# Optimization experiments

Hardware: AMD Instinct MI355X
Metric: run time of the kernel (lower is better)

Reference implementation:

```python
import jax, jax.numpy as jnp
import numpy as np

NB, HD, NL, NF = 5, 64, 4, 10           # num_bins, hidden_dim(d_model), num_layers, num_frames
DI, DS, DC, DTR = 128, 16, 4, 4          # d_inner=2*HD, d_state, d_conv, dt_rank=ceil(HD/16)
B, H, W = 4, 64, 64


def _conv2d(x, w, b):
    y = jax.lax.conv_general_dilated(x, w, (1, 1), 'SAME',
                                     dimension_numbers=('NCHW', 'OIHW', 'NCHW'))
    return y + b[None, :, None, None]


def _bn_relu(x, gamma, beta, eps=1e-5):
    # BatchNorm2d in training mode: biased batch stats over (N,H,W)
    mean = x.mean(axis=(0, 2, 3), keepdims=True)
    var = x.var(axis=(0, 2, 3), keepdims=True)
    y = (x - mean) * jax.lax.rsqrt(var + eps)
    return jax.nn.relu(y * gamma[None, :, None, None] + beta[None, :, None, None])


def _silu(x):
    return x * jax.nn.sigmoid(x)


def _causal_dwconv(x, w, b):
    # x: (B,L,DI), w: (DI,K) depthwise causal conv, b: (DI,)
    K = w.shape[1]
    L = x.shape[1]
    xp = jnp.pad(x, ((0, 0), (K - 1, 0), (0, 0)))
    y = sum(xp[:, k:k + L, :] * w[:, k] for k in range(K))
    return y + b


def _selective_scan(u, delta, A, Bm, Cm, D):
    # u,delta: (B,L,DI); A: (DI,DS); Bm,Cm: (B,L,DS); D: (DI,)
    dT, BT, CT, uT = (t.transpose(1, 0, 2) for t in (delta, Bm, Cm, u))
    h0 = jnp.zeros((u.shape[0], A.shape[0], A.shape[1]), u.dtype)

    def step(h, inp):
        d_t, B_t, C_t, u_t = inp                     # (B,DI),(B,DS),(B,DS),(B,DI)
        dA = jnp.exp(d_t[:, :, None] * A)            # (B,DI,DS)
        h = dA * h + (d_t * u_t)[:, :, None] * B_t[:, None, :]
        y = jnp.einsum('bds,bs->bd', h, C_t)
        return h, y

    _, ys = jax.lax.scan(step, h0, (dT, BT, CT, uT))  # ys: (L,B,DI)
    return ys.transpose(1, 0, 2) + u * D


def _mamba(x, in_proj, conv_w, conv_b, x_proj, dt_w, dt_b, A_log, Dp, out_proj):
    xz = x @ in_proj.T                               # (B,L,2*DI)
    xi, z = jnp.split(xz, 2, axis=-1)
    xi = _silu(_causal_dwconv(xi, conv_w, conv_b))
    xdbc = xi @ x_proj.T                             # (B,L,DTR+2*DS)
    dt, Bm, Cm = jnp.split(xdbc, [DTR, DTR + DS], axis=-1)
    delta = jax.nn.softplus(dt @ dt_w.T + dt_b)
    A = -jnp.exp(A_log)
    y = _selective_scan(xi, delta, A, Bm, Cm, Dp)
    return (y * _silu(z)) @ out_proj.T


def setup_inputs() -> dict:
    key = jax.random.key(0)
    ks = jax.random.split(key, 20)
    s = 0.02
    inp = {
        'x': jax.random.normal(ks[0], (B, NB, H, W), jnp.float32),
        'enc_w': jax.random.normal(ks[1], (HD, NB, 3, 3), jnp.float32) * s,
        'enc_b': jnp.zeros((HD,), jnp.float32),
        'enc_g': jnp.ones((HD,), jnp.float32),
        'enc_be': jnp.zeros((HD,), jnp.float32),
        'in_proj': jax.random.normal(ks[2], (NL, 2 * DI, HD), jnp.float32) * s,
        'conv_w': jax.random.normal(ks[3], (NL, DI, DC), jnp.float32) * s,
        'conv_b': jnp.zeros((NL, DI), jnp.float32),
        'x_proj': jax.random.normal(ks[4], (NL, DTR + 2 * DS, DI), jnp.float32) * s,
        'dt_w': jax.random.normal(ks[5], (NL, DI, DTR), jnp.float32) * s,
        'dt_b': jax.random.normal(ks[6], (NL, DI), jnp.float32) * 0.1 - 4.0,
        'A_log': jnp.broadcast_to(jnp.log(jnp.arange(1, DS + 1, dtype=jnp.float32)),
                                  (NL, DI, DS)).copy(),
        'Dp': jnp.ones((NL, DI), jnp.float32),
        'out_proj': jax.random.normal(ks[7], (NL, HD, DI), jnp.float32) * s,
        'dec1_w': jax.random.normal(ks[8], (HD, HD, 3, 3), jnp.float32) * s,
        'dec1_b': jnp.zeros((HD,), jnp.float32),
        'dec1_g': jnp.ones((HD,), jnp.float32),
        'dec1_be': jnp.zeros((HD,), jnp.float32),
        'dec2_w': jax.random.normal(ks[9], (NF, HD, 3, 3), jnp.float32) * s,
        'dec2_b': jnp.zeros((NF,), jnp.float32),
    }
    return inp


def reference(x, enc_w, enc_b, enc_g, enc_be, in_proj, conv_w, conv_b, x_proj,
              dt_w, dt_b, A_log, Dp, out_proj, dec1_w, dec1_b, dec1_g, dec1_be,
              dec2_w, dec2_b):
    Bb, _, Hh, Ww = x.shape
    h = _bn_relu(_conv2d(x, enc_w, enc_b), enc_g, enc_be)   # (B,HD,H,W)
    t = h.reshape(Bb, HD, Hh * Ww).transpose(0, 2, 1)        # (B,L,HD)
    for i in range(NL):
        t = t + _mamba(t, in_proj[i], conv_w[i], conv_b[i], x_proj[i],
                       dt_w[i], dt_b[i], A_log[i], Dp[i], out_proj[i])
    h = t.transpose(0, 2, 1).reshape(Bb, HD, Hh, Ww)
    h = _bn_relu(_conv2d(h, dec1_w, dec1_b), dec1_g, dec1_be)
    return _conv2d(h, dec2_w, dec2_b)                        # (B,NF,H,W)
```

## Files before the change

### kernel.cpp

```cpp
#include <hip/hip_runtime.h>
#include <hip/hip_bf16.h>

#define BB   4
#define NBC  5
#define HD   64
#define NLAYER 4
#define NFC  10
#define DIM  128
#define DSN  16
#define DCN  4
#define DTRK 4
#define HH   64
#define WWD  64
#define LL   4096
#define MM   (BB*LL)
#define NCHUNK 128
#define CLEN   32
#define TSTEP  16

__global__ void k_enc_conv(const float* __restrict__ x, const float* __restrict__ w,
                           const float* __restrict__ bias, float* __restrict__ out) {
    int idx = blockIdx.x * blockDim.x + threadIdx.x;
    int wx = idx & 63;
    int hy = (idx >> 6) & 63;
    int co = (idx >> 12) & 63;
    int b  = idx >> 18;
    float acc = bias[co];
    for (int ci = 0; ci < NBC; ++ci) {
        const float* xin = x + (((long)(b * NBC + ci)) << 12);
        const float* wp  = w + (co * NBC + ci) * 9;
        #pragma unroll
        for (int kh = 0; kh < 3; ++kh) {
            int ih = hy + kh - 1;
            if (ih < 0 || ih >= HH) continue;
            #pragma unroll
            for (int kw = 0; kw < 3; ++kw) {
                int iw = wx + kw - 1;
                if (iw < 0 || iw >= WWD) continue;
                acc += xin[(ih << 6) + iw] * wp[kh * 3 + kw];
            }
        }
    }
    out[idx] = acc;
}

__global__ void k_bn_stats(const float* __restrict__ src, float* __restrict__ mv) {
    __shared__ float s1[256];
    __shared__ float s2[256];
    int c = blockIdx.x;
    int tid = threadIdx.x;
    float sum = 0.f, sq = 0.f;
    for (int i = tid; i < BB * LL; i += 256) {
        int b = i >> 12;
        int hw = i & 4095;
        float v = src[((long)((b << 6) + c) << 12) + hw];
        sum += v; sq += v * v;
    }
    s1[tid] = sum; s2[tid] = sq;
    __syncthreads();
    for (int off = 128; off > 0; off >>= 1) {
        if (tid < off) { s1[tid] += s1[tid + off]; s2[tid] += s2[tid + off]; }
        __syncthreads();
    }
    if (tid == 0) {
        float m = s1[0] * (1.f / 16384.f);
        mv[c] = m;
        mv[64 + c] = s2[0] * (1.f / 16384.f) - m * m;
    }
}

__global__ void k_bn_tr_seq(const float* __restrict__ src, const float* __restrict__ mv,
                            const float* __restrict__ g, const float* __restrict__ be,
                            float* __restrict__ tout) {
    __shared__ float s[64 * 65];
    int blk = blockIdx.x;
    int b = blk >> 6;
    int hw0 = (blk & 63) << 6;
    int tid = threadIdx.x;
    for (int i = tid; i < 4096; i += 256) {
        int pix = i & 63, c = i >> 6;
        s[c * 65 + pix] = src[((long)((b << 6) + c) << 12) + hw0 + pix];
    }
    __syncthreads();
    for (int i = tid; i < 4096; i += 256) {
        int c = i & 63, pix = i >> 6;
        float v = s[c * 65 + pix];
        float y = (v - mv[c]) * rsqrtf(mv[64 + c] + 1e-5f) * g[c] + be[c];
        tout[((long)((b << 12) + hw0 + pix) << 6) + c] = fmaxf(y, 0.f);
    }
}

__global__ void k_bn_stats_pm_part(const float* __restrict__ src, float* __restrict__ pbuf) {
    __shared__ float s1[256], s2[256];
    int g = blockIdx.x;
    int tid = threadIdx.x;
    int c = tid & 63;
    int p = tid >> 6;
    float sum = 0.f, sq = 0.f;
    for (int row = (g << 2) + p; row < MM; row += 256) {
        float v = src[(long)row * 64 + c];
        sum += v; sq += v * v;
    }
    s1[tid] = sum; s2[tid] = sq;
    __syncthreads();
    if (p == 0) {
        sum = s1[c] + s1[64 + c] + s1[128 + c] + s1[192 + c];
        sq  = s2[c] + s2[64 + c] + s2[128 + c] + s2[192 + c];
        pbuf[(g << 6) + c] = sum;
        pbuf[4096 + (g << 6) + c] = sq;
    }
}

__global__ void k_bn_stats_pm_fin(const float* __restrict__ pbuf, float* __restrict__ mv) {
    int c = threadIdx.x;
    float s = 0.f, q = 0.f;
    for (int g = 0; g < 64; ++g) {
        s += pbuf[(g << 6) + c];
        q += pbuf[4096 + (g << 6) + c];
    }
    float m = s * (1.f / 16384.f);
    mv[c] = m;
    mv[64 + c] = q * (1.f / 16384.f) - m * m;
}

__global__ void k_prep_wt(const float* __restrict__ in_proj, const float* __restrict__ out_proj,
                          float* __restrict__ wTin, float* __restrict__ wTout) {
    int idx = blockIdx.x * blockDim.x + threadIdx.x;
    if (idx < 65536) {
        int n = idx & 255, k = (idx >> 8) & 63, l = idx >> 14;
        wTin[idx] = in_proj[(l << 14) + (n << 6) + k];
    } else {
        int j = idx - 65536;
        int n = j & 63, k = (j >> 6) & 127, l = j >> 13;
        wTout[j] = out_proj[(l << 13) + (n << 7) + k];
    }
}

__global__ __launch_bounds__(256, 1) void k_gemm_in2(const float* __restrict__ tin,
                                                     const float* __restrict__ wT,
                                                     float* __restrict__ xz) {
    __shared__ __align__(16) float ts[64 * 68];
    long m0 = (long)blockIdx.x << 6;
    int tid = threadIdx.x;
    int rg = tid >> 5;
    int cg = tid & 31;
    for (int i = tid; i < 4096; i += 256) {
        int r = i >> 6, k = i & 63;
        ts[r * 68 + k] = tin[(m0 << 6) + i];
    }
    __syncthreads();
    float acc[8][8] = {};
    int n0 = cg << 3;
    for (int k4 = 0; k4 < 16; ++k4) {
        float4 a[8];
        #pragma unroll
        for (int r2 = 0; r2 < 8; ++r2)
            a[r2] = *(const float4*)&ts[((rg << 3) + r2) * 68 + (k4 << 2)];
        #pragma unroll
        for (int kk = 0; kk < 4; ++kk) {
            const float* wr = wT + (((k4 << 2) + kk) << 8) + n0;
            float4 w0 = *(const float4*)&wr[0];
            float4 w1 = *(const float4*)&wr[4];
            #pragma unroll
            for (int r2 = 0; r2 < 8; ++r2) {
                float av = (kk == 0) ? a[r2].x : (kk == 1) ? a[r2].y
                         : (kk == 2) ? a[r2].z : a[r2].w;
                acc[r2][0] += av * w0.x; acc[r2][1] += av * w0.y;
                acc[r2][2] += av * w0.z; acc[r2][3] += av * w0.w;
                acc[r2][4] += av * w1.x; acc[r2][5] += av * w1.y;
                acc[r2][6] += av * w1.z; acc[r2][7] += av * w1.w;
            }
        }
    }
    #pragma unroll
    for (int r2 = 0; r2 < 8; ++r2) {
        long m = m0 + (rg << 3) + r2;
        *(float4*)&xz[(m << 8) + n0]     = make_float4(acc[r2][0], acc[r2][1], acc[r2][2], acc[r2][3]);
        *(float4*)&xz[(m << 8) + n0 + 4] = make_float4(acc[r2][4], acc[r2][5], acc[r2][6], acc[r2][7]);
    }
}

__global__ void k_xproj_fused(const float* __restrict__ xz, const float* __restrict__ cw,
                              const float* __restrict__ cb, const float* __restrict__ Wx,
                              const float* __restrict__ dw, const float* __restrict__ dbias,
                              float* __restrict__ xi, float* __restrict__ xdbc,
                              float* __restrict__ delta) {
    __shared__ float xz_s[35 * 132];
    __shared__ float xi_s[32 * 132];
    __shared__ float w_s[36 * 132];
    __shared__ float xs[32 * 40];
    __shared__ float cwT[4 * 128];
    __shared__ float cb_s[128];
    long m0 = (long)blockIdx.x << 5;
    int l0 = (int)(m0 & 4095);
    int tid = threadIdx.x;

    for (int i = tid; i < 35 * 128; i += 256) {
        int j = i >> 7, k = i & 127;
        int l = l0 - 3 + j;
        float v = 0.f;
        if (l >= 0) v = xz[(m0 - 3 + j) * 256 + k];
        xz_s[j * 132 + k] = v;
    }
    if (tid < 128) cb_s[tid] = cb[tid];
    for (int i = tid; i < 512; i += 256) {
        int kk = i >> 7, di = i & 127;
        cwT[(kk << 7) + di] = cw[(di << 2) + kk];
    }
    for (int i = tid; i < 4608; i += 256) {
        int n = i >> 7, k = i & 127;
        w_s[n * 132 + k] = Wx[i];
// ... 21 lines not shown
    }
    __syncthreads();

    int n = tid & 63;
    int rg = tid >> 6;
    if (n < 36) {
        float acc[8] = {0,0,0,0,0,0,0,0};
        for (int k4 = 0; k4 < 32; ++k4) {
            float4 w4 = *(const float4*)&w_s[n * 132 + (k4 << 2)];
            #pragma unroll
            for (int r = 0; r < 8; ++r) {
                float4 a4 = *(const float4*)&xi_s[((rg << 3) + r) * 132 + (k4 << 2)];
                acc[r] += a4.x * w4.x + a4.y * w4.y + a4.z * w4.z + a4.w * w4.w;
            }
        }
        #pragma unroll
        for (int r = 0; r < 8; ++r) {
            int rr = (rg << 3) + r;
            xdbc[(m0 + rr) * 36 + n] = acc[r];
            xs[rr * 40 + n] = acc[r];
        }
    }
    __syncthreads();
    for (int i = tid; i < 4096; i += 256) {
        int r = i >> 7, di = i & 127;
        float v = dbias[di];
        float4 d4 = *(const float4*)&dw[di << 2];
        v += xs[r * 40 + 0] * d4.x + xs[r * 40 + 1] * d4.y
           + xs[r * 40 + 2] * d4.z + xs[r * 40 + 3] * d4.w;
        delta[(m0 + r) * 128 + di] = (v > 20.f) ? v : log1pf(expf(v));
    }
}

__global__ void k_scan_p1(const float* __restrict__ delta, const float* __restrict__ xi,
                          const float* __restrict__ xdbc, const float* __restrict__ A_log,
                          float* __restrict__ Pb, float* __restrict__ Sb) {
    __shared__ float d_s[TSTEP][64];
    __shared__ float u_s[TSTEP][64];
    __shared__ float b_s[TSTEP][16];
    int chunk = blockIdx.x, b = blockIdx.y, half = blockIdx.z;
    int tid = threadIdx.x;
    int dq = tid & 3;
    int dil = tid >> 2;
    int di = (half << 6) + dil;
    float4 al = *(const float4*)&A_log[(di << 4) + (dq << 2)];
    float Av[4] = { -expf(al.x), -expf(al.y), -expf(al.z), -expf(al.w) };
    float h[4] = {0.f, 0.f, 0.f, 0.f};
    float P[4] = {1.f, 1.f, 1.f, 1.f};
    long t0 = ((long)b << 12) + (long)chunk * CLEN;

    int srow = tid >> 4, sc4 = (tid & 15) << 2;
    for (int tile = 0; tile < CLEN / TSTEP; ++tile) {
        __syncthreads();
        long ls = t0 + tile * TSTEP + srow;
        *(float4*)&d_s[srow][sc4] = *(const float4*)&delta[(ls << 7) + (half << 6) + sc4];
        *(float4*)&u_s[srow][sc4] = *(const float4*)&xi[(ls << 7) + (half << 6) + sc4];
        if (tid < 64) {
            int r2 = tid >> 2, cc = (tid & 3) << 2;
            long l2 = t0 + tile * TSTEP + r2;
            *(float4*)&b_s[r2][cc] = *(const float4*)&xdbc[l2 * 36 + DTRK + cc];
        }
        __syncthreads();
        #pragma unroll
        for (int i = 0; i < TSTEP; ++i) {
            float d = d_s[i][dil];
            float u = u_s[i][dil];
            float du = d * u;
            float4 Bv = *(float4*)&b_s[i][dq << 2];
            float a0 = __expf(d * Av[0]); h[0] = a0 * h[0] + du * Bv.x; P[0] *= a0;
            float a1 = __expf(d * Av[1]); h[1] = a1 * h[1] + du * Bv.y; P[1] *= a1;
            float a2 = __expf(d * Av[2]); h[2] = a2 * h[2] + du * Bv.z; P[2] *= a2;
            float a3 = __expf(d * Av[3]); h[3] = a3 * h[3] + du * Bv.w; P[3] *= a3;
        }
    }
    long o = (((long)chunk * BB + b) << 11) + (di << 4) + (dq << 2);
    *(float4*)&Pb[o] = make_float4(P[0], P[1], P[2], P[3]);
    *(float4*)&Sb[o] = make_float4(h[0], h[1], h[2], h[3]);
}

__global__ void k_scan_p2(float* Pb, const float* __restrict__ Sb) {
    int t = blockIdx.x * blockDim.x + threadIdx.x;
    int b = t >> 11;
    int s = t & 2047;
    float h = 0.f;
    for (int c = 0; c < NCHUNK; ++c) {
        long idx = (((long)c * BB + b) << 11) + s;
        float p = Pb[idx];
        float sv = Sb[idx];
        Pb[idx] = h;
        h = p * h + sv;
    }
}

__global__ void k_scan_p3(const float* __restrict__ delta, const float* __restrict__ xi,
                          const float* __restrict__ xdbc, const float* __restrict__ A_log,
                          const float* __restrict__ Dp, const float* __restrict__ xz,
                          const float* __restrict__ hin, float* __restrict__ gated) {
    __shared__ float d_s[TSTEP][64];
    __shared__ float u_s[TSTEP][64];
    __shared__ float bc_s[TSTEP][32];
    __shared__ float y_s[TSTEP][64];
    int chunk = blockIdx.x, b = blockIdx.y, half = blockIdx.z;
    int tid = threadIdx.x;
    int dq = tid & 3;
    int dil = tid >> 2;
    int di = (half << 6) + dil;
    float4 al = *(const float4*)&A_log[(di << 4) + (dq << 2)];
    float Av[4] = { -expf(al.x), -expf(al.y), -expf(al.z), -expf(al.w) };
    float Dv = Dp[di];
    long ho = (((long)chunk * BB + b) << 11) + (di << 4) + (dq << 2);
    float4 h4 = *(const float4*)&hin[ho];
    float h[4] = { h4.x, h4.y, h4.z, h4.w };
    long t0 = ((long)b << 12) + (long)chunk * CLEN;

    int srow = tid >> 4, sc4 = (tid & 15) << 2;
    for (int tile = 0; tile < CLEN / TSTEP; ++tile) {
        __syncthreads();
        long ls = t0 + tile * TSTEP + srow;
        *(float4*)&d_s[srow][sc4] = *(const float4*)&delta[(ls << 7) + (half << 6) + sc4];
        *(float4*)&u_s[srow][sc4] = *(const float4*)&xi[(ls << 7) + (half << 6) + sc4];
        if (tid < 128) {
            int r2 = tid >> 3, cc = (tid & 7) << 2;
            long l2 = t0 + tile * TSTEP + r2;
            *(float4*)&bc_s[r2][cc] = *(const float4*)&xdbc[l2 * 36 + DTRK + cc];
        }
        __syncthreads();
        #pragma unroll
        for (int i = 0; i < TSTEP; ++i) {
            float d = d_s[i][dil];
            float u = u_s[i][dil];
            float du = d * u;
            float4 Bv = *(float4*)&bc_s[i][dq << 2];
            float4 Cv = *(float4*)&bc_s[i][16 + (dq << 2)];
            float a0 = __expf(d * Av[0]); h[0] = a0 * h[0] + du * Bv.x;
            float a1 = __expf(d * Av[1]); h[1] = a1 * h[1] + du * Bv.y;
            float a2 = __expf(d * Av[2]); h[2] = a2 * h[2] + du * Bv.z;
            float a3 = __expf(d * Av[3]); h[3] = a3 * h[3] + du * Bv.w;
            float yp = h[0] * Cv.x + h[1] * Cv.y + h[2] * Cv.z + h[3] * Cv.w;
            yp += __shfl_xor(yp, 1);
            yp += __shfl_xor(yp, 2);
            if (dq == 0)
                y_s[i][dil] = yp + u * Dv;
        }
        __syncthreads();
        {
            long l = t0 + tile * TSTEP + srow;
            float4 y4 = *(float4*)&y_s[srow][sc4];
            float4 z4 = *(const float4*)&xz[(l << 8) + DIM + (half << 6) + sc4];
            float4 o;
            o.x = y4.x * (z4.x / (1.f + __expf(-z4.x)));
            o.y = y4.y * (z4.y / (1.f + __expf(-z4.y)));
            o.z = y4.z * (z4.z / (1.f + __expf(-z4.z)));
            o.w = y4.w * (z4.w / (1.f + __expf(-z4.w)));
            *(float4*)&gated[(l << 7) + (half << 6) + sc4] = o;
        }
    }
}

__global__ __launch_bounds__(256, 1) void k_gemm_out2(const float* __restrict__ gated,
                                                      const float* __restrict__ wT,
                                                      float* __restrict__ tio) {
    __shared__ __align__(16) float ts[64 * 132];
    long m0 = (long)blockIdx.x << 6;
    int tid = threadIdx.x;
    int rg = tid >> 4;
    int cg = tid & 15;
    for (int i = tid; i < 8192; i += 256) {
        int r2 = i >> 7, k = i & 127;
        ts[r2 * 132 + k] = gated[(m0 << 7) + i];
    }
    __syncthreads();
    float acc[4][4] = {};
    int n0 = cg << 2;
    for (int k4 = 0; k4 < 32; ++k4) {
        float4 a[4];
        #pragma unroll
        for (int r2 = 0; r2 < 4; ++r2)
            a[r2] = *(const float4*)&ts[((rg << 2) + r2) * 132 + (k4 << 2)];
        #pragma unroll
        for (int kk = 0; kk < 4; ++kk) {
            const float* wr = wT + (((k4 << 2) + kk) << 6) + n0;
            float4 w0 = *(const float4*)&wr[0];
            #pragma unroll
            for (int r2 = 0; r2 < 4; ++r2) {
                float av = (kk == 0) ? a[r2].x : (kk == 1) ? a[r2].y
                         : (kk == 2) ? a[r2].z : a[r2].w;
                acc[r2][0] += av * w0.x; acc[r2][1] += av * w0.y;
                acc[r2][2] += av * w0.z; acc[r2][3] += av * w0.w;
            }
        }
    }
    #pragma unroll
    for (int r2 = 0; r2 < 4; ++r2) {
        long m = m0 + (rg << 2) + r2;
        float4 t0 = *(const float4*)&tio[(m << 6) + n0];
        t0.x += acc[r2][0]; t0.y += acc[r2][1];
        t0.z += acc[r2][2]; t0.w += acc[r2][3];
        *(float4*)&tio[(m << 6) + n0] = t0;
    }
}

__global__ void k_prep_wdec1(const float* __restrict__ w, float* __restrict__ wT) {
    int idx = blockIdx.x * blockDim.x + threadIdx.x;
    int co = idx & 63;
    int tap = (idx >> 6) % 9;
    int ci = idx / 576;
    wT[idx] = w[co * 576 + ci * 9 + tap];
}

__global__ void k_prep_wdec2(const float* __restrict__ w, float* __restrict__ wT) {
    int idx = blockIdx.x * blockDim.x + threadIdx.x;
    if (idx >= 64 * NFC * 12) return;
    int tap = idx % 12;
    int t2 = idx / 12;
    int co = t2 % NFC;
    int ci = t2 / NFC;
    wT[idx] = (tap < 9) ? w[co * 576 + ci * 9 + tap] : 0.f;
}

__global__ __launch_bounds__(256, 1) void k_dec1_new(const float* __restrict__ tin,
                                                     const float* __restrict__ wT,
                                                     const float* __restrict__ bias,
                                                     float* __restrict__ out) {
    __shared__ __align__(16) float x_s[64 * 132];
    __shared__ __align__(16) float w_s[4 * 4608];
    int tile = blockIdx.x;
    int b = blockIdx.y;
    int ty0 = (tile >> 3) << 3;
    int tx0 = (tile & 7) << 3;
    int tid = threadIdx.x;
    int wv = tid >> 6;
    int lane = tid & 63;
    int r = lane >> 3;
    int cg = lane & 7;

    for (int i = tid; i < 6400; i += 256) {
        int pl = i >> 6;
        int c = i & 63;
        int py = pl / 10, px = pl - py * 10;
        int ih = ty0 + py - 1, iw = tx0 + px - 1;
        float v = 0.f;
        if (ih >= 0 && ih < HH && iw >= 0 && iw < WWD)
            v = tin[(((long)((b << 12) + (ih << 6) + iw)) << 6) + c];
        x_s[c * 132 + py * 12 + px] = v;
    }
    float* myw = &w_s[wv * 4608];
    const float* gw = wT + (wv * 16) * 576;
    float4 pref[18];
    #pragma unroll
    for (int i = 0; i < 18; ++i)
        pref[i] = *(const float4*)&gw[(i * 64 + lane) * 4];
    #pragma unroll
    for (int i = 0; i < 18; ++i)
        *(float4*)&myw[(i * 64 + lane) * 4] = pref[i];
    __syncthreads();

// ... 23 lines not shown
            #pragma unroll
            for (int kh = 0; kh < 3; ++kh) {
                #pragma unroll
                for (int kw = 0; kw < 3; ++kw) {
                    const float* wp2 = wp + (kh * 3 + kw) * 64 + (cg << 3);
                    float4 wa = *(const float4*)&wp2[0];
                    float4 wb = *(const float4*)&wp2[4];
                    #pragma unroll
                    for (int j = 0; j < 8; ++j) {
                        float xv = xrow[kh][kw + j];
                        acc[j][0] += xv * wa.x; acc[j][1] += xv * wa.y;
                        acc[j][2] += xv * wa.z; acc[j][3] += xv * wa.w;
                        acc[j][4] += xv * wb.x; acc[j][5] += xv * wb.y;
                        acc[j][6] += xv * wb.z; acc[j][7] += xv * wb.w;
                    }
                }
            }
        }
        if (ch == 0) {
            #pragma unroll
            for (int i = 0; i < 18; ++i)
                *(float4*)&myw[(i * 64 + lane) * 4] = pref[i];
        }
    }

    #pragma unroll
    for (int j = 0; j < 8; ++j) {
        *(float4*)&myw[lane * 68 + (j << 3)]     = make_float4(acc[j][0], acc[j][1], acc[j][2], acc[j][3]);
        *(float4*)&myw[lane * 68 + (j << 3) + 4] = make_float4(acc[j][4], acc[j][5], acc[j][6], acc[j][7]);
    }
    __syncthreads();

    float bv = bias[lane];
    #pragma unroll
    for (int pp = 0; pp < 16; ++pp) {
        int pr = (wv << 1) + (pp >> 3);
        int pc = pp & 7;
        int ol = (pr << 3) + (lane >> 3);
        int ix = (pc << 3) + (lane & 7);
        float s = w_s[ol * 68 + ix] + w_s[4608 + ol * 68 + ix]
                + w_s[9216 + ol * 68 + ix] + w_s[13824 + ol * 68 + ix] + bv;
        out[(((long)((b << 12) + ((ty0 + pr) << 6) + tx0 + pc)) << 6) + lane] = s;
    }
}

__global__ void k_dec2_fused(const float* __restrict__ src, const float* __restrict__ mv,
                             const float* __restrict__ g, const float* __restrict__ be,
                             const float* __restrict__ wT, const float* __restrict__ bias,
                             float* __restrict__ out) {
    __shared__ float x_s[64 * 101];
    __shared__ float w_s[64 * NFC * 12];
    __shared__ float sc_s[64];
    __shared__ float sh_s[64];
    int tile = blockIdx.x;
    int b = blockIdx.y;
    int ty0 = (tile >> 3) << 3;
    int tx0 = (tile & 7) << 3;
    int tid = threadIdx.x;

    if (tid < 64) {
        float m = mv[tid], v = mv[64 + tid];
        float s = g[tid] * rsqrtf(v + 1e-5f);
        sc_s[tid] = s;
        sh_s[tid] = be[tid] - m * s;
    }
    for (int i = tid; i < 64 * NFC * 12; i += 256)
        w_s[i] = wT[i];
    __syncthreads();

    for (int i = tid; i < 6400; i += 256) {
        int pl = i >> 6;
        int c = i & 63;
        int py = pl / 10, px = pl - py * 10;
        int ih = ty0 + py - 1, iw = tx0 + px - 1;
        float v = 0.f;
        if (ih >= 0 && ih < HH && iw >= 0 && iw < WWD) {
            v = src[((long)((b << 12) + (ih << 6) + iw)) * 64 + c];
            v = fmaxf(v * sc_s[c] + sh_s[c], 0.f);
        }
        x_s[c * 101 + pl] = v;
    }
    __syncthreads();

    int px = tid & 63;
    int py = px >> 3, pxx = px & 7;
    int cog = tid >> 6;
    float acc[3] = {0.f, 0.f, 0.f};
    int nco = (cog < 2) ? 3 : 2;

    for (int ci = 0; ci < 64; ++ci) {
        const float* xr = &x_s[ci * 101 + py * 10 + pxx];
        float xv[9];
        #pragma unroll
        for (int kh = 0; kh < 3; ++kh)
            #pragma unroll
// ... 19 lines not shown
        int co = cog + (j << 2);
        out[((long)(b * NFC + co) << 12) + hw] = acc[j] + bias[co];
    }
}

extern "C" void kernel_launch(void* const* d_in, const int* in_sizes, int n_in,
                              void* d_out, int out_size, void* d_ws, size_t ws_size,
                              hipStream_t stream) {
    const float* x       = (const float*)d_in[0];
    const float* enc_w   = (const float*)d_in[1];
    const float* enc_b   = (const float*)d_in[2];
    const float* enc_g   = (const float*)d_in[3];
    const float* enc_be  = (const float*)d_in[4];
    const float* in_proj = (const float*)d_in[5];
    const float* conv_w  = (const float*)d_in[6];
    const float* conv_b  = (const float*)d_in[7];
    const float* x_proj  = (const float*)d_in[8];
    const float* dt_w    = (const float*)d_in[9];
    const float* dt_b    = (const float*)d_in[10];
    const float* A_log   = (const float*)d_in[11];
    const float* Dp      = (const float*)d_in[12];
    const float* out_prj = (const float*)d_in[13];
    const float* dec1_w  = (const float*)d_in[14];
    const float* dec1_b  = (const float*)d_in[15];
    const float* dec1_g  = (const float*)d_in[16];
    const float* dec1_be = (const float*)d_in[17];
    const float* dec2_w  = (const float*)d_in[18];
    const float* dec2_b  = (const float*)d_in[19];
    float* out = (float*)d_out;

    float* ws = (float*)d_ws;
    size_t off = 0;
    float* conv_buf  = ws + off; off += 1048576;
    float* mv        = ws + off; off += 128;
    float* pbuf      = ws + off; off += 8192;
    float* wT1       = ws + off; off += 36864;
    float* wT2       = ws + off; off += 7680;
    float* wTin      = ws + off; off += 65536;
    float* wTout     = ws + off; off += 32768;
    float* t_buf     = ws + off; off += 1048576;
    float* xz_buf    = ws + off; off += 4194304;
    float* xi_buf    = ws + off; off += 2097152;
    float* xdbc_buf  = ws + off; off += 589824;
    float* delta_buf = ws + off; off += 2097152;
    float* gated_buf = ws + off; off += 2097152;
    (void)ws_size; (void)in_sizes; (void)n_in; (void)out_size;

    float* Pb = conv_buf;
    float* Sb = gated_buf;

    k_prep_wt<<<384, 256, 0, stream>>>(in_proj, out_prj, wTin, wTout);
    k_prep_wdec1<<<144, 256, 0, stream>>>(dec1_w, wT1);
    k_prep_wdec2<<<30, 256, 0, stream>>>(dec2_w, wT2);

    k_enc_conv<<<4096, 256, 0, stream>>>(x, enc_w, enc_b, conv_buf);
    k_bn_stats<<<64, 256, 0, stream>>>(conv_buf, mv);
    k_bn_tr_seq<<<256, 256, 0, stream>>>(conv_buf, mv, enc_g, enc_be, t_buf);

    dim3 sg(NCHUNK, BB, 2);
    for (int i = 0; i < NLAYER; ++i) {
        k_gemm_in2<<<256, 256, 0, stream>>>(t_buf, wTin + i * 16384, xz_buf);
        k_xproj_fused<<<512, 256, 0, stream>>>(xz_buf, conv_w + i * DIM * DCN,
                                               conv_b + i * DIM, x_proj + i * 36 * DIM,
                                               dt_w + i * DIM * DTRK, dt_b + i * DIM,
                                               xi_buf, xdbc_buf, delta_buf);
        k_scan_p1<<<sg, 256, 0, stream>>>(delta_buf, xi_buf, xdbc_buf,
                                          A_log + i * DIM * DSN, Pb, Sb);
        k_scan_p2<<<32, 256, 0, stream>>>(Pb, Sb);
        k_scan_p3<<<sg, 256, 0, stream>>>(delta_buf, xi_buf, xdbc_buf,
                                          A_log + i * DIM * DSN, Dp + i * DIM,
                                          xz_buf, Pb, gated_buf);
        k_gemm_out2<<<256, 256, 0, stream>>>(gated_buf, wTout + i * 8192, t_buf);
    }

    dim3 dg1(64, BB);
    k_dec1_new<<<dg1, 256, 0, stream>>>(t_buf, wT1, dec1_b, conv_buf);
    k_bn_stats_pm_part<<<64, 256, 0, stream>>>(conv_buf, pbuf);
    k_bn_stats_pm_fin<<<1, 64, 0, stream>>>(pbuf, mv);
    k_dec2_fused<<<dg1, 256, 0, stream>>>(conv_buf, mv, dec1_g, dec1_be, wT2, dec2_b, out);
}
```

Baseline: 565.8 us.

## Fuse scan phases with grid barriers, fold BN stats into convs, merge GEMMs

Merges the three selective-scan kernels into one persistent kernel that uses atomic-counter grid barriers, so it relies on all 1024 blocks being co-resident. Batch-norm statistics are now accumulated with atomics inside the encoder and dec1 convolutions, which removes separate reduction passes. The out-projection GEMM is fused with the next layer's in-projection GEMM, and the weight-prep kernels are merged into one. The goal is fewer launches and less global traffic. The risks are deadlock if occupancy falls short, contention on the atomics, and run-to-run differences in float summation order.

```diff
diff --git a/kernel.cpp b/kernel.cpp
--- a/kernel.cpp
+++ b/kernel.cpp
@@ -17,10 +17,56 @@
 #define NCHUNK 128
 #define CLEN   32
 #define TSTEP  16
+#define NBLK_SCAN 1024
+
+__device__ __forceinline__ void gbar(int* c, int n) {
+    __threadfence();
+    __syncthreads();
+    if (threadIdx.x == 0) {
+        atomicAdd(c, 1);
+        while (atomicAdd(c, 0) < n)
+            __builtin_amdgcn_s_sleep(16);
+        __threadfence();
+    }
+    __syncthreads();
+}
+
+__global__ void k_prep_all(const float* __restrict__ in_proj, const float* __restrict__ out_proj,
+                           const float* __restrict__ dec1_w, const float* __restrict__ dec2_w,
+                           float* __restrict__ wTin, float* __restrict__ wTout,
+                           float* __restrict__ wT1, float* __restrict__ wT2,
+                           float* __restrict__ stats, float* __restrict__ stats2,
+                           int* __restrict__ sync) {
+    int idx = blockIdx.x * blockDim.x + threadIdx.x;
+    if (idx < 65536) {
+        int n = idx & 255, k = (idx >> 8) & 63, l = idx >> 14;
+        wTin[idx] = in_proj[(l << 14) + (n << 6) + k];
+    } else if (idx < 98304) {
+        int j = idx - 65536;
+        int n = j & 63, k = (j >> 6) & 127, l = j >> 13;
+        wTout[j] = out_proj[(l << 13) + (n << 7) + k];
+    } else if (idx < 135168) {
+        int j = idx - 98304;
+        int co = j & 63, tap = (j >> 6) % 9, ci = j / 576;
+        wT1[j] = dec1_w[co * 576 + ci * 9 + tap];
+    } else if (idx < 142848) {
+        int j = idx - 135168;
+        int tap = j % 12, t2 = j / 12, co = t2 % NFC, ci = t2 / NFC;
+        wT2[j] = (tap < 9) ? dec2_w[co * 576 + ci * 9 + tap] : 0.f;
+    } else if (idx < 143104) {
+        int j = idx - 142848;
+        if (j < 128) stats[j] = 0.f; else stats2[j - 128] = 0.f;
+    } else if (idx < 143168) {
+        sync[idx - 143104] = 0;
+    }
+}
 
 __global__ void k_enc_conv(const float* __restrict__ x, const float* __restrict__ w,
-                           const float* __restrict__ bias, float* __restrict__ out) {
-    int idx = blockIdx.x * blockDim.x + threadIdx.x;
+                           const float* __restrict__ bias, float* __restrict__ out,
+                           float* __restrict__ stats) {
+    __shared__ float r1[256], r2[256];
+    int tid = threadIdx.x;
+    int idx = blockIdx.x * 256 + tid;
     int wx = idx & 63;
     int hy = (idx >> 6) & 63;
     int co = (idx >> 12) & 63;
@@ -42,41 +88,33 @@
         }
     }
     out[idx] = acc;
-}
-
-__global__ void k_bn_stats(const float* __restrict__ src, float* __restrict__ mv) {
-    __shared__ float s1[256];
-    __shared__ float s2[256];
-    int c = blockIdx.x;
-    int tid = threadIdx.x;
-    float sum = 0.f, sq = 0.f;
-    for (int i = tid; i < BB * LL; i += 256) {
-        int b = i >> 12;
-        int hw = i & 4095;
-        float v = src[((long)((b << 6) + c) << 12) + hw];
-        sum += v; sq += v * v;
-    }
-    s1[tid] = sum; s2[tid] = sq;
+    r1[tid] = acc; r2[tid] = acc * acc;
     __syncthreads();
     for (int off = 128; off > 0; off >>= 1) {
-        if (tid < off) { s1[tid] += s1[tid + off]; s2[tid] += s2[tid + off]; }
+        if (tid < off) { r1[tid] += r1[tid + off]; r2[tid] += r2[tid + off]; }
         __syncthreads();
     }
     if (tid == 0) {
-        float m = s1[0] * (1.f / 16384.f);
-        mv[c] = m;
-        mv[64 + c] = s2[0] * (1.f / 16384.f) - m * m;
-    }
-}
-
-__global__ void k_bn_tr_seq(const float* __restrict__ src, const float* __restrict__ mv,
+        atomicAdd(&stats[co], r1[0]);
+        atomicAdd(&stats[64 + co], r2[0]);
+    }
+}
+
+__global__ void k_bn_tr_seq(const float* __restrict__ src, const float* __restrict__ stats,
                             const float* __restrict__ g, const float* __restrict__ be,
                             float* __restrict__ tout) {
     __shared__ float s[64 * 65];
+    __shared__ float sc[64], sh[64];
     int blk = blockIdx.x;
     int b = blk >> 6;
     int hw0 = (blk & 63) << 6;
     int tid = threadIdx.x;
+    if (tid < 64) {
+        float m = stats[tid] * (1.f / 16384.f);
+        float var = stats[64 + tid] * (1.f / 16384.f) - m * m;
+        float ss = g[tid] * rsqrtf(var + 1e-5f);
+        sc[tid] = ss; sh[tid] = be[tid] - m * ss;
+    }
     for (int i = tid; i < 4096; i += 256) {
         int pix = i & 63, c = i >> 6;
         s[c * 65 + pix] = src[((long)((b << 6) + c) << 12) + hw0 + pix];
@@ -84,55 +122,8 @@
     __syncthreads();
     for (int i = tid; i < 4096; i += 256) {
         int c = i & 63, pix = i >> 6;
-        float v = s[c * 65 + pix];
-        float y = (v - mv[c]) * rsqrtf(mv[64 + c] + 1e-5f) * g[c] + be[c];
+        float y = s[c * 65 + pix] * sc[c] + sh[c];
         tout[((long)((b << 12) + hw0 + pix) << 6) + c] = fmaxf(y, 0.f);
-    }
-}
-
-__global__ void k_bn_stats_pm_part(const float* __restrict__ src, float* __restrict__ pbuf) {
-    __shared__ float s1[256], s2[256];
-    int g = blockIdx.x;
-    int tid = threadIdx.x;
-    int c = tid & 63;
-    int p = tid >> 6;
-    float sum = 0.f, sq = 0.f;
-    for (int row = (g << 2) + p; row < MM; row += 256) {
-        float v = src[(long)row * 64 + c];
-        sum += v; sq += v * v;
-    }
-    s1[tid] = sum; s2[tid] = sq;
-    __syncthreads();
-    if (p == 0) {
-        sum = s1[c] + s1[64 + c] + s1[128 + c] + s1[192 + c];
-        sq  = s2[c] + s2[64 + c] + s2[128 + c] + s2[192 + c];
-        pbuf[(g << 6) + c] = sum;
-        pbuf[4096 + (g << 6) + c] = sq;
-    }
-}
-
-__global__ void k_bn_stats_pm_fin(const float* __restrict__ pbuf, float* __restrict__ mv) {
-    int c = threadIdx.x;
-    float s = 0.f, q = 0.f;
-    for (int g = 0; g < 64; ++g) {
-        s += pbuf[(g << 6) + c];
-        q += pbuf[4096 + (g << 6) + c];
-    }
-    float m = s * (1.f / 16384.f);
-    mv[c] = m;
-    mv[64 + c] = q * (1.f / 16384.f) - m * m;
-}
-
-__global__ void k_prep_wt(const float* __restrict__ in_proj, const float* __restrict__ out_proj,
-                          float* __restrict__ wTin, float* __restrict__ wTout) {
-    int idx = blockIdx.x * blockDim.x + threadIdx.x;
-    if (idx < 65536) {
-        int n = idx & 255, k = (idx >> 8) & 63, l = idx >> 14;
-        wTin[idx] = in_proj[(l << 14) + (n << 6) + k];
-    } else {
-        int j = idx - 65536;
-        int n = j & 63, k = (j >> 6) & 127, l = j >> 13;
-        wTout[j] = out_proj[(l << 13) + (n << 7) + k];
     }
 }
 
@@ -177,6 +168,130 @@
         long m = m0 + (rg << 3) + r2;
         *(float4*)&xz[(m << 8) + n0]     = make_float4(acc[r2][0], acc[r2][1], acc[r2][2], acc[r2][3]);
         *(float4*)&xz[(m << 8) + n0 + 4] = make_float4(acc[r2][4], acc[r2][5], acc[r2][6], acc[r2][7]);
+    }
+}
+
+__global__ __launch_bounds__(256, 1) void k_gemm_oi(const float* __restrict__ gated,
+                                                    const float* __restrict__ wTo,
+                                                    const float* __restrict__ wTi,
+                                                    float* __restrict__ tio,
+                                                    float* __restrict__ xz) {
+    __shared__ __align__(16) float g_s[64 * 132];
+    __shared__ __align__(16) float t_s[64 * 68];
+    long m0 = (long)blockIdx.x << 6;
+    int tid = threadIdx.x;
+    for (int i = tid; i < 8192; i += 256) {
+        int r = i >> 7, k = i & 127;
+        g_s[r * 132 + k] = gated[(m0 << 7) + i];
+    }
+    __syncthreads();
+    {
+        int rg = tid >> 4, cg = tid & 15;
+        int n0 = cg << 2;
+        float acc[4][4] = {};
+        for (int k4 = 0; k4 < 32; ++k4) {
+            float4 a[4];
+            #pragma unroll
+            for (int r2 = 0; r2 < 4; ++r2)
+                a[r2] = *(const float4*)&g_s[((rg << 2) + r2) * 132 + (k4 << 2)];
+            #pragma unroll
+            for (int kk = 0; kk < 4; ++kk) {
+                const float* wr = wTo + (((k4 << 2) + kk) << 6) + n0;
+                float4 w0 = *(const float4*)&wr[0];
+                #pragma unroll
+                for (int r2 = 0; r2 < 4; ++r2) {
+                    float av = (kk == 0) ? a[r2].x : (kk == 1) ? a[r2].y
+                             : (kk == 2) ? a[r2].z : a[r2].w;
+                    acc[r2][0] += av * w0.x; acc[r2][1] += av * w0.y;
+                    acc[r2][2] += av * w0.z; acc[r2][3] += av * w0.w;
+                }
+            }
+        }
+        #pragma unroll
+        for (int r2 = 0; r2 < 4; ++r2) {
+            long m = m0 + (rg << 2) + r2;
+            float4 t0 = *(const float4*)&tio[(m << 6) + n0];
+            t0.x += acc[r2][0]; t0.y += acc[r2][1];
+            t0.z += acc[r2][2]; t0.w += acc[r2][3];
+            *(float4*)&tio[(m << 6) + n0] = t0;
+            *(float4*)&t_s[((rg << 2) + r2) * 68 + n0] = t0;
+        }
+    }
+    __syncthreads();
+    {
+        int rg = tid >> 5, cg = tid & 31;
+        int n0 = cg << 3;
+        float acc[8][8] = {};
+        for (int k4 = 0; k4 < 16; ++k4) {
+            float4 a[8];
+            #pragma unroll
+            for (int r2 = 0; r2 < 8; ++r2)
+                a[r2] = *(const float4*)&t_s[((rg << 3) + r2) * 68 + (k4 << 2)];
+            #pragma unroll
+            for (int kk = 0; kk < 4; ++kk) {
+                const float* wr = wTi + (((k4 << 2) + kk) << 8) + n0;
+                float4 w0 = *(const float4*)&wr[0];
+                float4 w1 = *(const float4*)&wr[4];
+                #pragma unroll
+                for (int r2 = 0; r2 < 8; ++r2) {
+                    float av = (kk == 0) ? a[r2].x : (kk == 1) ? a[r2].y
+                             : (kk == 2) ? a[r2].z : a[r2].w;
+                    acc[r2][0] += av * w0.x; acc[r2][1] += av * w0.y;
+                    acc[r2][2] += av * w0.z; acc[r2][3] += av * w0.w;
+                    acc[r2][4] += av * w1.x; acc[r2][5] += av * w1.y;
+                    acc[r2][6] += av * w1.z; acc[r2][7] += av * w1.w;
+                }
+            }
+        }
+        #pragma unroll
+        for (int r2 = 0; r2 < 8; ++r2) {
+            long m = m0 + (rg << 3) + r2;
+            *(float4*)&xz[(m << 8) + n0]     = make_float4(acc[r2][0], acc[r2][1], acc[r2][2], acc[r2][3]);
+            *(float4*)&xz[(m << 8) + n0 + 4] = make_float4(acc[r2][4], acc[r2][5], acc[r2][6], acc[r2][7]);
+        }
+    }
+}
+
+__global__ __launch_bounds__(256, 1) void k_gemm_out2(const float* __restrict__ gated,
+                                                      const float* __restrict__ wT,
+                                                      float* __restrict__ tio) {
+    __shared__ __align__(16) float ts[64 * 132];
+    long m0 = (long)blockIdx.x << 6;
+    int tid = threadIdx.x;
+    int rg = tid >> 4;
+    int cg = tid & 15;
+    for (int i = tid; i < 8192; i += 256) {
+        int r2 = i >> 7, k = i & 127;
+        ts[r2 * 132 + k] = gated[(m0 << 7) + i];
+    }
+    __syncthreads();
+    float acc[4][4] = {};
+    int n0 = cg << 2;
+    for (int k4 = 0; k4 < 32; ++k4) {
+        float4 a[4];
+        #pragma unroll
+        for (int r2 = 0; r2 < 4; ++r2)
+            a[r2] = *(const float4*)&ts[((rg << 2) + r2) * 132 + (k4 << 2)];
+        #pragma unroll
+        for (int kk = 0; kk < 4; ++kk) {
+            const float* wr = wT + (((k4 << 2) + kk) << 6) + n0;
+            float4 w0 = *(const float4*)&wr[0];
+            #pragma unroll
+            for (int r2 = 0; r2 < 4; ++r2) {
+                float av = (kk == 0) ? a[r2].x : (kk == 1) ? a[r2].y
+                         : (kk == 2) ? a[r2].z : a[r2].w;
+                acc[r2][0] += av * w0.x; acc[r2][1] += av * w0.y;
+                acc[r2][2] += av * w0.z; acc[r2][3] += av * w0.w;
+            }
+        }
+    }
+    #pragma unroll
+    for (int r2 = 0; r2 < 4; ++r2) {
+        long m = m0 + (rg << 2) + r2;
+        float4 t0 = *(const float4*)&tio[(m << 6) + n0];
+        t0.x += acc[r2][0]; t0.y += acc[r2][1];
+        t0.z += acc[r2][2]; t0.w += acc[r2][3];
+        *(float4*)&tio[(m << 6) + n0] = t0;
     }
 }
 
@@ -264,12 +379,15 @@
     }
 }
 
-__global__ void k_scan_p1(const float* __restrict__ delta, const float* __restrict__ xi,
-                          const float* __restrict__ xdbc, const float* __restrict__ A_log,
-                          float* __restrict__ Pb, float* __restrict__ Sb) {
+__global__ __launch_bounds__(256, 4) void k_scan(
+        const float* __restrict__ delta, const float* __restrict__ xi,
+        const float* __restrict__ xdbc, const float* __restrict__ A_log,
+        const float* __restrict__ Dp, const float* __restrict__ xz,
+        float* Pb, float* Sb, float* __restrict__ gated, int* sync) {
     __shared__ float d_s[TSTEP][64];
     __shared__ float u_s[TSTEP][64];
-    __shared__ float b_s[TSTEP][16];
+    __shared__ float bc_s[TSTEP][32];
+    __shared__ float y_s[TSTEP][64];
     int chunk = blockIdx.x, b = blockIdx.y, half = blockIdx.z;
     int tid = threadIdx.x;
     int dq = tid & 3;
@@ -277,183 +395,112 @@
     int di = (half << 6) + dil;
     float4 al = *(const float4*)&A_log[(di << 4) + (dq << 2)];
     float Av[4] = { -expf(al.x), -expf(al.y), -expf(al.z), -expf(al.w) };
-    float h[4] = {0.f, 0.f, 0.f, 0.f};
-    float P[4] = {1.f, 1.f, 1.f, 1.f};
     long t0 = ((long)b << 12) + (long)chunk * CLEN;
-
     int srow = tid >> 4, sc4 = (tid & 15) << 2;
-    for (int tile = 0; tile < CLEN / TSTEP; ++tile) {
-        __syncthreads();
-        long ls = t0 + tile * TSTEP + srow;
-        *(float4*)&d_s[srow][sc4] = *(const float4*)&delta[(ls << 7) + (half << 6) + sc4];
-        *(float4*)&u_s[srow][sc4] = *(const float4*)&xi[(ls << 7) + (half << 6) + sc4];
-        if (tid < 64) {
-            int r2 = tid >> 2, cc = (tid & 3) << 2;
-            long l2 = t0 + tile * TSTEP + r2;
-            *(float4*)&b_s[r2][cc] = *(const float4*)&xdbc[l2 * 36 + DTRK + cc];
-        }
-        __syncthreads();
-        #pragma unroll
-        for (int i = 0; i < TSTEP; ++i) {
-            float d = d_s[i][dil];
-            float u = u_s[i][dil];
-            float du = d * u;
-            float4 Bv = *(float4*)&b_s[i][dq << 2];
-            float a0 = __expf(d * Av[0]); h[0] = a0 * h[0] + du * Bv.x; P[0] *= a0;
-            float a1 = __expf(d * Av[1]); h[1] = a1 * h[1] + du * Bv.y; P[1] *= a1;
-            float a2 = __expf(d * Av[2]); h[2] = a2 * h[2] + du * Bv.z; P[2] *= a2;
-            float a3 = __expf(d * Av[3]); h[3] = a3 * h[3] + du * Bv.w; P[3] *= a3;
-        }
-    }
     long o = (((long)chunk * BB + b) << 11) + (di << 4) + (dq << 2);
-    *(float4*)&Pb[o] = make_float4(P[0], P[1], P[2], P[3]);
-    *(float4*)&Sb[o] = make_float4(h[0], h[1], h[2], h[3]);
-}
-
-__global__ void k_scan_p2(float* Pb, const float* __restrict__ Sb) {
-    int t = blockIdx.x * blockDim.x + threadIdx.x;
-    int b = t >> 11;
-    int s = t & 2047;
-    float h = 0.f;
-    for (int c = 0; c < NCHUNK; ++c) {
-        long idx = (((long)c * BB + b) << 11) + s;
-        float p = Pb[idx];
-        float sv = Sb[idx];
-        Pb[idx] = h;
-        h = p * h + sv;
-    }
-}
-
-__global__ void k_scan_p3(const float* __restrict__ delta, const float* __restrict__ xi,
-                          const float* __restrict__ xdbc, const float* __restrict__ A_log,
-                          const float* __restrict__ Dp, const float* __restrict__ xz,
-                          const float* __restrict__ hin, float* __restrict__ gated) {
-    __shared__ float d_s[TSTEP][64];
-    __shared__ float u_s[TSTEP][64];
-    __shared__ float bc_s[TSTEP][32];
-    __shared__ float y_s[TSTEP][64];
-    int chunk = blockIdx.x, b = blockIdx.y, half = blockIdx.z;
-    int tid = threadIdx.x;
-    int dq = tid & 3;
-    int dil = tid >> 2;
-    int di = (half << 6) + dil;
-    float4 al = *(const float4*)&A_log[(di << 4) + (dq << 2)];
-    float Av[4] = { -expf(al.x), -expf(al.y), -expf(al.z), -expf(al.w) };
-    float Dv = Dp[di];
-    long ho = (((long)chunk * BB + b) << 11) + (di << 4) + (dq << 2);
-    float4 h4 = *(const float4*)&hin[ho];
-    float h[4] = { h4.x, h4.y, h4.z, h4.w };
-    long t0 = ((long)b << 12) + (long)chunk * CLEN;
-
-    int srow = tid >> 4, sc4 = (tid & 15) << 2;
-    for (int tile = 0; tile < CLEN / TSTEP; ++tile) {
-        __syncthreads();
-        long ls = t0 + tile * TSTEP + srow;
-        *(float4*)&d_s[srow][sc4] = *(const float4*)&delta[(ls << 7) + (half << 6) + sc4];
-        *(float4*)&u_s[srow][sc4] = *(const float4*)&xi[(ls << 7) + (half << 6) + sc4];
-        if (tid < 128) {
-            int r2 = tid >> 3, cc = (tid & 7) << 2;
-            long l2 = t0 + tile * TSTEP + r2;
-            *(float4*)&bc_s[r2][cc] = *(const float4*)&xdbc[l2 * 36 + DTRK + cc];
-        }
-        __syncthreads();
-        #pragma unroll
-        for (int i = 0; i < TSTEP; ++i) {
-            float d = d_s[i][dil];
-            float u = u_s[i][dil];
-            float du = d * u;
-            float4 Bv = *(float4*)&bc_s[i][dq << 2];
-            float4 Cv = *(float4*)&bc_s[i][16 + (dq << 2)];
-            float a0 = __expf(d * Av[0]); h[0] = a0 * h[0] + du * Bv.x;
-            float a1 = __expf(d * Av[1]); h[1] = a1 * h[1] + du * Bv.y;
-            float a2 = __expf(d * Av[2]); h[2] = a2 * h[2] + du * Bv.z;
-            float a3 = __expf(d * Av[3]); h[3] = a3 * h[3] + du * Bv.w;
-            float yp = h[0] * Cv.x + h[1] * Cv.y + h[2] * Cv.z + h[3] * Cv.w;
-            yp += __shfl_xor(yp, 1);
-            yp += __shfl_xor(yp, 2);
-            if (dq == 0)
-                y_s[i][dil] = yp + u * Dv;
-        }
-        __syncthreads();
-        {
-            long l = t0 + tile * TSTEP + srow;
-            float4 y4 = *(float4*)&y_s[srow][sc4];
-            float4 z4 = *(const float4*)&xz[(l << 8) + DIM + (half << 6) + sc4];
-            float4 o;
-            o.x = y4.x * (z4.x / (1.f + __expf(-z4.x)));
-            o.y = y4.y * (z4.y / (1.f + __expf(-z4.y)));
-            o.z = y4.z * (z4.z / (1.f + __expf(-z4.z)));
-            o.w = y4.w * (z4.w / (1.f + __expf(-z4.w)));
-            *(float4*)&gated[(l << 7) + (half << 6) + sc4] = o;
-        }
-    }
-}
-
-__global__ __launch_bounds__(256, 1) void k_gemm_out2(const float* __restrict__ gated,
-                                                      const float* __restrict__ wT,
-                                                      float* __restrict__ tio) {
-    __shared__ __align__(16) float ts[64 * 132];
-    long m0 = (long)blockIdx.x << 6;
-    int tid = threadIdx.x;
-    int rg = tid >> 4;
-    int cg = tid & 15;
-    for (int i = tid; i < 8192; i += 256) {
-        int r2 = i >> 7, k = i & 127;
-        ts[r2 * 132 + k] = gated[(m0 << 7) + i];
-    }
-    __syncthreads();
-    float acc[4][4] = {};
-    int n0 = cg << 2;
-    for (int k4 = 0; k4 < 32; ++k4) {
-        float4 a[4];
-        #pragma unroll
-        for (int r2 = 0; r2 < 4; ++r2)
-            a[r2] = *(const float4*)&ts[((rg << 2) + r2) * 132 + (k4 << 2)];
-        #pragma unroll
-        for (int kk = 0; kk < 4; ++kk) {
-            const float* wr = wT + (((k4 << 2) + kk) << 6) + n0;
-            float4 w0 = *(const float4*)&wr[0];
-            #pragma unroll
-            for (int r2 = 0; r2 < 4; ++r2) {
-                float av = (kk == 0) ? a[r2].x : (kk == 1) ? a[r2].y
-                         : (kk == 2) ? a[r2].z : a[r2].w;
-                acc[r2][0] += av * w0.x; acc[r2][1] += av * w0.y;
-                acc[r2][2] += av * w0.z; acc[r2][3] += av * w0.w;
-            }
-        }
-    }
-    #pragma unroll
-    for (int r2 = 0; r2 < 4; ++r2) {
-        long m = m0 + (rg << 2) + r2;
-        float4 t0 = *(const float4*)&tio[(m << 6) + n0];
-        t0.x += acc[r2][0]; t0.y += acc[r2][1];
-        t0.z += acc[r2][2]; t0.w += acc[r2][3];
-        *(float4*)&tio[(m << 6) + n0] = t0;
-    }
-}
-
-__global__ void k_prep_wdec1(const float* __restrict__ w, float* __restrict__ wT) {
-    int idx = blockIdx.x * blockDim.x + threadIdx.x;
-    int co = idx & 63;
-    int tap = (idx >> 6) % 9;
-    int ci = idx / 576;
-    wT[idx] = w[co * 576 + ci * 9 + tap];
-}
-
-__global__ void k_prep_wdec2(const float* __restrict__ w, float* __restrict__ wT) {
-    int idx = blockIdx.x * blockDim.x + threadIdx.x;
-    if (idx >= 64 * NFC * 12) return;
-    int tap = idx % 12;
-    int t2 = idx / 12;
-    int co = t2 % NFC;
-    int ci = t2 / NFC;
-    wT[idx] = (tap < 9) ? w[co * 576 + ci * 9 + tap] : 0.f;
+
+    {
+        float h[4] = {0.f, 0.f, 0.f, 0.f};
+        float P[4] = {1.f, 1.f, 1.f, 1.f};
+        for (int tile = 0; tile < CLEN / TSTEP; ++tile) {
+            __syncthreads();
+            long ls = t0 + tile * TSTEP + srow;
+            *(float4*)&d_s[srow][sc4] = *(const float4*)&delta[(ls << 7) + (half << 6) + sc4];
+            *(float4*)&u_s[srow][sc4] = *(const float4*)&xi[(ls << 7) + (half << 6) + sc4];
+            if (tid < 64) {
+                int r2 = tid >> 2, cc = (tid & 3) << 2;
+                long l2 = t0 + tile * TSTEP + r2;
+                *(float4*)&bc_s[r2][cc] = *(const float4*)&xdbc[l2 * 36 + DTRK + cc];
+            }
+            __syncthreads();
+            #pragma unroll
+            for (int i = 0; i < TSTEP; ++i) {
+                float d = d_s[i][dil];
+                float u = u_s[i][dil];
+                float du = d * u;
+                float4 Bv = *(float4*)&bc_s[i][dq << 2];
+                float a0 = __expf(d * Av[0]); h[0] = a0 * h[0] + du * Bv.x; P[0] *= a0;
+                float a1 = __expf(d * Av[1]); h[1] = a1 * h[1] + du * Bv.y; P[1] *= a1;
+                float a2 = __expf(d * Av[2]); h[2] = a2 * h[2] + du * Bv.z; P[2] *= a2;
+                float a3 = __expf(d * Av[3]); h[3] = a3 * h[3] + du * Bv.w; P[3] *= a3;
+            }
+        }
+        *(float4*)&Pb[o] = make_float4(P[0], P[1], P[2], P[3]);
+        *(float4*)&Sb[o] = make_float4(h[0], h[1], h[2], h[3]);
+    }
+    gbar(sync, NBLK_SCAN);
+
+    {
+        int flat = blockIdx.x + (blockIdx.y << 7) + (blockIdx.z << 9);
+        if (flat < 32) {
+            int t = (flat << 8) + tid;
+            int bb = t >> 11;
+            int s = t & 2047;
+            float h = 0.f;
+            for (int c = 0; c < NCHUNK; ++c) {
+                long idx2 = (((long)c * BB + bb) << 11) + s;
+                float p = Pb[idx2];
+                float sv = Sb[idx2];
+                Pb[idx2] = h;
+                h = p * h + sv;
+            }
+        }
+    }
+    gbar(sync + 1, NBLK_SCAN);
+
+    {
+        float Dv = Dp[di];
+        float4 h4 = *(const float4*)&Pb[o];
+        float h[4] = { h4.x, h4.y, h4.z, h4.w };
+        for (int tile = 0; tile < CLEN / TSTEP; ++tile) {
+            __syncthreads();
+            long ls = t0 + tile * TSTEP + srow;
+            *(float4*)&d_s[srow][sc4] = *(const float4*)&delta[(ls << 7) + (half << 6) + sc4];
+            *(float4*)&u_s[srow][sc4] = *(const float4*)&xi[(ls << 7) + (half << 6) + sc4];
+            if (tid < 128) {
+                int r2 = tid >> 3, cc = (tid & 7) << 2;
+                long l2 = t0 + tile * TSTEP + r2;
+                *(float4*)&bc_s[r2][cc] = *(const float4*)&xdbc[l2 * 36 + DTRK + cc];
+            }
+            __syncthreads();
+            #pragma unroll
+            for (int i = 0; i < TSTEP; ++i) {
+                float d = d_s[i][dil];
+                float u = u_s[i][dil];
+                float du = d * u;
+                float4 Bv = *(float4*)&bc_s[i][dq << 2];
+                float4 Cv = *(float4*)&bc_s[i][16 + (dq << 2)];
+                float a0 = __expf(d * Av[0]); h[0] = a0 * h[0] + du * Bv.x;
+                float a1 = __expf(d * Av[1]); h[1] = a1 * h[1] + du * Bv.y;
+                float a2 = __expf(d * Av[2]); h[2] = a2 * h[2] + du * Bv.z;
+                float a3 = __expf(d * Av[3]); h[3] = a3 * h[3] + du * Bv.w;
+                float yp = h[0] * Cv.x + h[1] * Cv.y + h[2] * Cv.z + h[3] * Cv.w;
+                yp += __shfl_xor(yp, 1);
+                yp += __shfl_xor(yp, 2);
+                if (dq == 0)
+                    y_s[i][dil] = yp + u * Dv;
+            }
+            __syncthreads();
+            {
+                long l = t0 + tile * TSTEP + srow;
+                float4 y4 = *(float4*)&y_s[srow][sc4];
+                float4 z4 = *(const float4*)&xz[(l << 8) + DIM + (half << 6) + sc4];
+                float4 og;
+                og.x = y4.x * (z4.x / (1.f + __expf(-z4.x)));
+                og.y = y4.y * (z4.y / (1.f + __expf(-z4.y)));
+                og.z = y4.z * (z4.z / (1.f + __expf(-z4.z)));
+                og.w = y4.w * (z4.w / (1.f + __expf(-z4.w)));
+                *(float4*)&gated[(l << 7) + (half << 6) + sc4] = og;
+            }
+        }
+    }
 }
 
 __global__ __launch_bounds__(256, 1) void k_dec1_new(const float* __restrict__ tin,
                                                      const float* __restrict__ wT,
                                                      const float* __restrict__ bias,
-                                                     float* __restrict__ out) {
+                                                     float* __restrict__ out,
+                                                     float* __restrict__ stats2) {
     __shared__ __align__(16) float x_s[64 * 132];
     __shared__ __align__(16) float w_s[4 * 4608];
     int tile = blockIdx.x;
@@ -543,6 +590,7 @@
     __syncthreads();
 
     float bv = bias[lane];
+    float ssum = 0.f, ssq = 0.f;
     #pragma unroll
     for (int pp = 0; pp < 16; ++pp) {
         int pr = (wv << 1) + (pp >> 3);
@@ -552,10 +600,21 @@
         float s = w_s[ol * 68 + ix] + w_s[4608 + ol * 68 + ix]
                 + w_s[9216 + ol * 68 + ix] + w_s[13824 + ol * 68 + ix] + bv;
         out[(((long)((b << 12) + ((ty0 + pr) << 6) + tx0 + pc)) << 6) + lane] = s;
-    }
-}
-
-__global__ void k_dec2_fused(const float* __restrict__ src, const float* __restrict__ mv,
+        ssum += s; ssq += s * s;
+    }
+    float* red = x_s;
+    red[(wv << 6) + lane] = ssum;
+    red[256 + (wv << 6) + lane] = ssq;
+    __syncthreads();
+    if (tid < 64) {
+        float a = red[tid] + red[64 + tid] + red[128 + tid] + red[192 + tid];
+        float q = red[256 + tid] + red[320 + tid] + red[384 + tid] + red[448 + tid];
+        atomicAdd(&stats2[tid], a);
+        atomicAdd(&stats2[64 + tid], q);
+    }
+}
+
+__global__ void k_dec2_fused(const float* __restrict__ src, const float* __restrict__ stats2,
                              const float* __restrict__ g, const float* __restrict__ be,
                              const float* __restrict__ wT, const float* __restrict__ bias,
                              float* __restrict__ out) {
@@ -570,8 +629,9 @@
     int tid = threadIdx.x;
 
     if (tid < 64) {
-        float m = mv[tid], v = mv[64 + tid];
-        float s = g[tid] * rsqrtf(v + 1e-5f);
+        float m = stats2[tid] * (1.f / 16384.f);
+        float var = stats2[64 + tid] * (1.f / 16384.f) - m * m;
+        float s = g[tid] * rsqrtf(var + 1e-5f);
         sc_s[tid] = s;
         sh_s[tid] = be[tid] - m * s;
     }
@@ -657,8 +717,9 @@
     float* ws = (float*)d_ws;
     size_t off = 0;
     float* conv_buf  = ws + off; off += 1048576;
-    float* mv        = ws + off; off += 128;
-    float* pbuf      = ws + off; off += 8192;
+    float* stats     = ws + off; off += 128;
+    float* stats2    = ws + off; off += 128;
+    float* syncf     = ws + off; off += 64;
     float* wT1       = ws + off; off += 36864;
     float* wT2       = ws + off; off += 7680;
     float* wTin      = ws + off; off += 65536;
@@ -671,36 +732,33 @@
     float* gated_buf = ws + off; off += 2097152;
     (void)ws_size; (void)in_sizes; (void)n_in; (void)out_size;
 
+    int* syncbuf = (int*)syncf;
     float* Pb = conv_buf;
     float* Sb = gated_buf;
 
-    k_prep_wt<<<384, 256, 0, stream>>>(in_proj, out_prj, wTin, wTout);
-    k_prep_wdec1<<<144, 256, 0, stream>>>(dec1_w, wT1);
-    k_prep_wdec2<<<30, 256, 0, stream>>>(dec2_w, wT2);
-
-    k_enc_conv<<<4096, 256, 0, stream>>>(x, enc_w, enc_b, conv_buf);
-    k_bn_stats<<<64, 256, 0, stream>>>(conv_buf, mv);
-    k_bn_tr_seq<<<256, 256, 0, stream>>>(conv_buf, mv, enc_g, enc_be, t_buf);
+    k_prep_all<<<560, 256, 0, stream>>>(in_proj, out_prj, dec1_w, dec2_w,
+                                        wTin, wTout, wT1, wT2, stats, stats2, syncbuf);
+
+    k_enc_conv<<<4096, 256, 0, stream>>>(x, enc_w, enc_b, conv_buf, stats);
+    k_bn_tr_seq<<<256, 256, 0, stream>>>(conv_buf, stats, enc_g, enc_be, t_buf);
 
     dim3 sg(NCHUNK, BB, 2);
+    k_gemm_in2<<<256, 256, 0, stream>>>(t_buf, wTin, xz_buf);
     for (int i = 0; i < NLAYER; ++i) {
-        k_gemm_in2<<<256, 256, 0, stream>>>(t_buf, wTin + i * 16384, xz_buf);
         k_xproj_fused<<<512, 256, 0, stream>>>(xz_buf, conv_w + i * DIM * DCN,
                                                conv_b + i * DIM, x_proj + i * 36 * DIM,
                                                dt_w + i * DIM * DTRK, dt_b + i * DIM,
                                                xi_buf, xdbc_buf, delta_buf);
-        k_scan_p1<<<sg, 256, 0, stream>>>(delta_buf, xi_buf, xdbc_buf,
-                                          A_log + i * DIM * DSN, Pb, Sb);
-        k_scan_p2<<<32, 256, 0, stream>>>(Pb, Sb);
-        k_scan_p3<<<sg, 256, 0, stream>>>(delta_buf, xi_buf, xdbc_buf,
-                                          A_log + i * DIM * DSN, Dp + i * DIM,
-                                          xz_buf, Pb, gated_buf);
-        k_gemm_out2<<<256, 256, 0, stream>>>(gated_buf, wTout + i * 8192, t_buf);
-    }
+        k_scan<<<sg, 256, 0, stream>>>(delta_buf, xi_buf, xdbc_buf,
+                                       A_log + i * DIM * DSN, Dp + i * DIM,
+                                       xz_buf, Pb, Sb, gated_buf, syncbuf + i * 2);
+        if (i < NLAYER - 1)
+            k_gemm_oi<<<256, 256, 0, stream>>>(gated_buf, wTout + i * 8192,
+                                               wTin + (i + 1) * 16384, t_buf, xz_buf);
+    }
+    k_gemm_out2<<<256, 256, 0, stream>>>(gated_buf, wTout + 3 * 8192, t_buf);
 
     dim3 dg1(64, BB);
-    k_dec1_new<<<dg1, 256, 0, stream>>>(t_buf, wT1, dec1_b, conv_buf);
-    k_bn_stats_pm_part<<<64, 256, 0, stream>>>(conv_buf, pbuf);
-    k_bn_stats_pm_fin<<<1, 64, 0, stream>>>(pbuf, mv);
-    k_dec2_fused<<<dg1, 256, 0, stream>>>(conv_buf, mv, dec1_g, dec1_be, wT2, dec2_b, out);
-}
+    k_dec1_new<<<dg1, 256, 0, stream>>>(t_buf, wT1, dec1_b, conv_buf, stats2);
+    k_dec2_fused<<<dg1, 256, 0, stream>>>(conv_buf, stats2, dec1_g, dec1_be, wT2, dec2_b, out);
+}
```

Result: slower. 1.716 ms (+203.3%).
